# Performance work log

Measured on AMD Instinct MI355X. Metric: run time of the kernel, lower is better.

Reference implementation:

```python
import math
import jax, jax.numpy as jnp
import numpy as np

# Frozen random shifts from the original module's __init__ (random.randint(-1,1))
SHIFT_C = 1   # p_2_0_1: roll along channel dim
SHIFT_H = 1   # p_4_1_0: roll along h
SHIFT_W = -1  # p_4_1_1: roll along w
K = 7         # horizontal window size (F.unfold kernel (1,7), padding (0,3))


def setup_inputs() -> dict:
    key = jax.random.key(0)
    k1, k2 = jax.random.split(key)
    n, c, h, w = 8, 256, 56, 56
    x = jax.random.normal(k1, (n, c, h, w), dtype=jnp.float32)
    # p_1_w ~ trunc_normal(std=0.1) around 1.0; approximate with 1 + 0.1*normal
    p1w = 1.0 + 0.1 * jax.random.normal(k2, (1, c, h, w), dtype=jnp.float32)
    return {"x": x, "p1w": p1w}


def _unfold_w7(t):
    # t: (n,c,h,w) -> (n,c,7,h,w): 7 horizontal taps, zero-padded (pad=3)
    w = t.shape[-1]
    tp = jnp.pad(t, ((0, 0), (0, 0), (0, 0), (3, 3)))
    return jnp.stack([tp[..., j:j + w] for j in range(K)], axis=2)


def reference(x, p1w):
    n, c, h, w = x.shape
    hw = h * w
    t1 = p1w * x                              # (n,c,h,w)
    t2 = jnp.roll(t1, SHIFT_C, axis=1)        # roll channels
    t3 = _unfold_w7(t2)                       # (n,c,7,h,w)
    t4 = jnp.roll(jnp.roll(t3, SHIFT_H, axis=3), SHIFT_W, axis=4)
    t5 = t1[:, :, None] - t3                  # (n,c,7,h,w)
    t6 = x[:, :, None] + t4                   # (n,c,7,h,w)
    x2 = x.reshape(n, c, hw)
    t5r = t5.reshape(n, c, K, hw)
    t6r = t6.reshape(n, c, K, hw)
    # scores: bmm(x (n,c,hw), t5^T (n,hw,c*7)) -> (n,c,c,7)
    t7 = jnp.einsum('nip,njkp->nijk', x2, t5r) / math.sqrt(hw)
    # aggregate: bmm(t7 (n,c,c*7), t6 (n,c*7,hw)) -> (n,c,hw)
    t8 = jnp.einsum('nijk,njkp->nip', t7, t6r) / math.sqrt(c * K)
    return t8.reshape(n, c, h, w)
```

## Files before the change

kernel.cpp:

```cpp
#include <hip/hip_runtime.h>

typedef unsigned short u16;
typedef __bf16 bf16x8 __attribute__((ext_vector_type(8)));
typedef float f32x4 __attribute__((ext_vector_type(4)));

#define HH  56
#define WW  56
#define HW  3136
#define CC  256
#define NB  8
#define CKP 2048
#define KS1 4

__device__ __forceinline__ u16 f2bf(float f) {
  unsigned int u = __float_as_uint(f);
  u += 0x7fffu + ((u >> 16) & 1u);
  return (u16)(u >> 16);
}
__device__ __forceinline__ float bf2f(u16 v) {
  return __uint_as_float((unsigned)v << 16);
}

__device__ __forceinline__ void lds_load16(const void* g, void* l) {
  __builtin_amdgcn_global_load_lds(
      (const __attribute__((address_space(1))) void*)g,
      (__attribute__((address_space(3))) void*)l, 16, 0, 0);
}

__global__ void pass1(const float* __restrict__ x, const float* __restrict__ p1w,
                      u16* __restrict__ t1b, u16* __restrict__ xb) {
  int i = blockIdx.x * 256 + threadIdx.x;
  int cw = i % (CC * HW / 4);
  float4 xv = ((const float4*)x)[i];
  float4 wv = ((const float4*)p1w)[cw];
  uint2 xo = make_uint2((unsigned)f2bf(xv.x) | ((unsigned)f2bf(xv.y) << 16),
                        (unsigned)f2bf(xv.z) | ((unsigned)f2bf(xv.w) << 16));
  ((uint2*)xb)[i] = xo;
  uint2 to = make_uint2((unsigned)f2bf(xv.x * wv.x) | ((unsigned)f2bf(xv.y * wv.y) << 16),
                        (unsigned)f2bf(xv.z * wv.z) | ((unsigned)f2bf(xv.w * wv.w) << 16));
  ((uint2*)t1b)[i] = to;
}

__global__ __launch_bounds__(256)
void gemm1f(const u16* __restrict__ A, const u16* __restrict__ t1b,
            float* __restrict__ Cp) {
  __shared__ u16 As[128 * 64];
  __shared__ u16 Bs[128 * 64];

  const int bi = blockIdx.x;
  const int nb = bi & 7;
  const int r  = bi >> 3;
  const int ks = r & 3;
  const int r2 = r >> 2;
  const int m0b = r2 & 1;
  const int n0b = r2 >> 1;

  const int it0 = 49 * ks / KS1, it1 = 49 * (ks + 1) / KS1;
  const u16* Ab  = A   + (long)nb * CC * HW;
  const u16* t1n = t1b + (long)nb * CC * HW;
  const int m0 = m0b * 128, n0 = n0b * 128;
  const int jb = n0b * 16;
  const int t = threadIdx.x;
  const int lane = t & 63, wave = t >> 6;
  const int wm = wave & 1, wn = wave >> 1;
  const int lm = lane & 15, quad = lane >> 4;

  const int jl = (t >> 3) & 15, pc = t & 7, hf = t >> 7;
  const int j  = jb + jl;
  const int jm = (j + CC - 1) & (CC - 1);
  const u16* arow = t1n + (long)j  * HW;
  const u16* wrow = t1n + (long)jm * HW;

  f32x4 acc[4][4];
#pragma unroll
  for (int a = 0; a < 4; ++a)
#pragma unroll
    for (int b = 0; b < 4; ++b) acc[a][b] = (f32x4)0.0f;

  int rowc[4], colc[4];
#pragma unroll
  for (int ci = 0; ci < 4; ++ci) {
    int c = t + ci * 256;
    rowc[ci] = c >> 3;
    colc[ci] = ((c & 7) ^ (rowc[ci] & 7)) * 8;
  }

  for (int it = it0; it < it1; ++it) {
    const int k0 = it * 64;
#pragma unroll
    for (int ci = 0; ci < 4; ++ci)
      lds_load16(Ab + (long)(m0 + rowc[ci]) * HW + k0 + colc[ci],
                 &As[(t + ci * 256) * 8]);

    {
      const int p8 = k0 + pc * 8;
      __attribute__((aligned(16))) u16 Ar[8];
      __attribute__((aligned(16))) u16 Wd[24];
      *(uint4*)Ar = *(const uint4*)&arow[p8];
#pragma unroll
      for (int L = 0; L < 3; ++L) {
        int ad = p8 - 8 + L * 8;
        ad = ad < 0 ? 0 : (ad > HW - 8 ? HW - 8 : ad);
        *(uint4*)&Wd[L * 8] = *(const uint4*)&wrow[ad];
      }
      const int w0t = p8 % 56;
      int wv[8];
#pragma unroll
      for (int e = 0; e < 8; ++e) { int w = w0t + e; wv[e] = w >= 56 ? w - 56 : w; }
      if (hf == 0) {
#pragma unroll
        for (int k = 0; k < 4; ++k) {
          __attribute__((aligned(16))) u16 v[8];
#pragma unroll
          for (int e = 0; e < 8; ++e)
            v[e] = ((unsigned)(wv[e] + k - 3) < 56u) ? Wd[e + k + 5] : (u16)0;
          *(uint4*)&Bs[(jl * 8 + k) * 64 + (pc ^ k) * 8] = *(const uint4*)v;
        }
      } else {
#pragma unroll
        for (int k = 4; k < 7; ++k) {
          __attribute__((aligned(16))) u16 v[8];
#pragma unroll
          for (int e = 0; e < 8; ++e)
            v[e] = ((unsigned)(wv[e] + k - 3) < 56u) ? Wd[e + k + 5] : (u16)0;
          *(uint4*)&Bs[(jl * 8 + k) * 64 + (pc ^ k) * 8] = *(const uint4*)v;
        }
        *(uint4*)&Bs[(jl * 8 + 7) * 64 + (pc ^ 7) * 8] = *(const uint4*)Ar;
      }
    }
    __syncthreads();
#pragma unroll
    for (int kk = 0; kk < 2; ++kk) {
      const int phys = ((kk * 4 + quad) ^ (lm & 7)) * 8;
      bf16x8 af[4], bv[4];
#pragma unroll
      for (int mi = 0; mi < 4; ++mi)
        af[mi] = *(const bf16x8*)&As[(wm * 64 + mi * 16 + lm) * 64 + phys];
#pragma unroll
      for (int ni = 0; ni < 4; ++ni)
        bv[ni] = *(const bf16x8*)&Bs[(wn * 64 + ni * 16 + lm) * 64 + phys];
#pragma unroll
      for (int mi = 0; mi < 4; ++mi)
#pragma unroll
        for (int ni = 0; ni < 4; ++ni)
          acc[mi][ni] = __builtin_amdgcn_mfma_f32_16x16x32_bf16(
              af[mi], bv[ni], acc[mi][ni], 0, 0, 0);
    }
    __syncthreads();
  }

  float* Cb = Cp + ((long)ks * NB + nb) * (long)CC * CKP;
#pragma unroll
  for (int mi = 0; mi < 4; ++mi)
#pragma unroll
    for (int ni = 0; ni < 4; ++ni) {
      int rb = m0 + wm * 64 + mi * 16 + quad * 4;
      int cg = n0 + wn * 64 + ni * 16 + lm;
#pragma unroll
      for (int r4 = 0; r4 < 4; ++r4)
        Cb[(long)(rb + r4) * CKP + cg] = acc[mi][ni][r4];
    }
}

__global__ void reduce1(const float* __restrict__ p1, u16* __restrict__ t7) {
  const int g = blockIdx.x * 256 + threadIdx.x;
  const long S = (long)NB * CC * CKP;
  const long base = (long)g * 8;
  float a[8];
#pragma unroll
  for (int e = 0; e < 8; ++e) a[e] = 0.0f;
#pragma unroll
  for (int ks = 0; ks < KS1; ++ks) {
    float4 lo = *(const float4*)&p1[ks * S + base];
    float4 hi = *(const float4*)&p1[ks * S + base + 4];
    a[0] += lo.x; a[1] += lo.y; a[2] += lo.z; a[3] += lo.w;
    a[4] += hi.x; a[5] += hi.y; a[6] += hi.z; a[7] += hi.w;
  }
  const float s = 1.0f / 56.0f;
  const float G = a[7];
  __attribute__((aligned(16))) u16 o[8];
  float s7 = 0.0f;
#pragma unroll
  for (int k = 0; k < 7; ++k) {
    float v = (G - a[k]) * s;
    s7 += v;
    o[k] = f2bf(v);
  }
  o[7] = f2bf(s7);
  *(uint4*)&t7[base] = *(const uint4*)o;
}

__global__ __launch_bounds__(256)
void gemm2f(const u16* __restrict__ A, const u16* __restrict__ xb,
            const u16* __restrict__ t1b, float* __restrict__ out) {
  __shared__ u16 As[128 * 64];
  __shared__ u16 Bs[64 * 64];

  const int bi = blockIdx.x;
  const int nb = bi & 7;
  const int r  = bi >> 3;
  const int m0b = r & 1;
  const int n0b = r >> 1;

  const u16* Ab  = A   + (long)nb * CC * CKP;
  const u16* xbn = xb  + (long)nb * CC * HW;
  const u16* t1n = t1b + (long)nb * CC * HW;
  const int m0 = m0b * 128, n0 = n0b * 64;
  const int t = threadIdx.x;
  const int lane = t & 63, wave = t >> 6;
  const int wm = wave & 1, wn = wave >> 1;
  const int lm = lane & 15, quad = lane >> 4;

  const int pr = t & 63, jg = t >> 6;
  const int p  = n0 + pr;
  const int h  = p / WW, w = p - h * WW;
  const int h2 = (h + HH - 1) % HH;
  const int w2 = (w + 1) % WW;
  const int swz = pr & 7;

  int toff[7], tmsk[7];
#pragma unroll
  for (int k = 0; k < 7; ++k) {
    int ww = w2 + k - 3;
    int wc = ww < 0 ? 0 : (ww > 55 ? 55 : ww);
    toff[k] = h2 * WW + wc;
    tmsk[k] = ((unsigned)ww < 56u);
  }

  f32x4 acc[4][2];
#pragma unroll
  for (int a = 0; a < 4; ++a)
#pragma unroll
    for (int b = 0; b < 2; ++b) acc[a][b] = (f32x4)0.0f;

  int rowc[4], colc[4];
#pragma unroll
  for (int ci = 0; ci < 4; ++ci) {
    int c = t + ci * 256;
    rowc[ci] = c >> 3;
    colc[ci] = ((c & 7) ^ (rowc[ci] & 7)) * 8;
  }

  for (int it = 0; it < 32; ++it) {
    const int k0 = it * 64;
#pragma unroll
    for (int ci = 0; ci < 4; ++ci)
      lds_load16(Ab + (long)(m0 + rowc[ci]) * CKP + k0 + colc[ci],
                 &As[(t + ci * 256) * 8]);

#pragma unroll
    for (int jj = 0; jj < 2; ++jj) {
      const int jch = it * 8 + jg * 2 + jj;
      const int jmm = (jch + CC - 1) & (CC - 1);
      const u16* trow = t1n + (long)jmm * HW;
      __attribute__((aligned(16))) u16 v[8];
#pragma unroll
      for (int k = 0; k < 7; ++k) {
        u16 tv = trow[toff[k]];
        v[k] = tmsk[k] ? tv : (u16)0;
      }
      v[7] = xbn[(long)jch * HW + p];
      *(uint4*)&Bs[pr * 64 + (((jg * 2 + jj) ^ swz) * 8)] = *(const uint4*)v;
    }
    __syncthreads();
#pragma unroll
    for (int kk = 0; kk < 2; ++kk) {
      const int phys = ((kk * 4 + quad) ^ (lm & 7)) * 8;
      bf16x8 af[4], bv[2];
#pragma unroll
      for (int mi = 0; mi < 4; ++mi)
        af[mi] = *(const bf16x8*)&As[(wm * 64 + mi * 16 + lm) * 64 + phys];
#pragma unroll
      for (int ni = 0; ni < 2; ++ni)
        bv[ni] = *(const bf16x8*)&Bs[(wn * 32 + ni * 16 + lm) * 64 + phys];
#pragma unroll
      for (int mi = 0; mi < 4; ++mi)
#pragma unroll
        for (int ni = 0; ni < 2; ++ni)
          acc[mi][ni] = __builtin_amdgcn_mfma_f32_16x16x32_bf16(
              af[mi], bv[ni], acc[mi][ni], 0, 0, 0);
    }
    __syncthreads();
  }

  const float s2 = 0.023622783f;
  float* Ob = out + (long)nb * CC * HW;
#pragma unroll
  for (int mi = 0; mi < 4; ++mi)
#pragma unroll
    for (int ni = 0; ni < 2; ++ni) {
      int rb = m0 + wm * 64 + mi * 16 + quad * 4;
      int cg = n0 + wn * 32 + ni * 16 + lm;
#pragma unroll
      for (int r4 = 0; r4 < 4; ++r4)
        Ob[(long)(rb + r4) * HW + cg] = acc[mi][ni][r4] * s2;
    }
}

extern "C" void kernel_launch(void* const* d_in, const int* in_sizes, int n_in,
                              void* d_out, int out_size, void* d_ws, size_t ws_size,
                              hipStream_t stream) {
  const float* x   = (const float*)d_in[0];
  const float* p1w = (const float*)d_in[1];

  char* ws = (char*)d_ws;
  size_t o = 0;
  u16* xb  = (u16*)(ws + o); o += (size_t)NB * CC * HW * 2;
  u16* t1b = (u16*)(ws + o); o += (size_t)NB * CC * HW * 2;
  u16* t7  = (u16*)(ws + o); o += (size_t)NB * CC * CKP * 2;
  float* p1 = (float*)(ws + o); o += (size_t)KS1 * NB * CC * CKP * 4;

  pass1<<<NB * CC * HW / 4 / 256, 256, 0, stream>>>(x, p1w, t1b, xb);
  gemm1f<<<NB * KS1 * 2 * 16, 256, 0, stream>>>(xb, t1b, p1);
  reduce1<<<NB * CC * CKP / 8 / 256, 256, 0, stream>>>(p1, t7);
  gemm2f<<<NB * 2 * 49, 256, 0, stream>>>(t7, xb, t1b, (float*)d_out);
}
```

Before: 185.6 us.

## Stage t1/x rows into double-buffered LDS via async DMA in gemm2f

Instead of each thread doing seven scattered 2-byte global loads per channel to build the unfolded B tile, two waves asynchronously copy the two needed source rows of t1 and the x slice into LDS with global_load_lds. The stage for the next iteration is double-buffered, and the B tile is then assembled from LDS. This is meant to replace uncoalesced global gathers with coalesced 16-byte DMA and to overlap them with compute. The cost is more LDS, more complex indexing that assumes a 64-pixel tile spans at most two image rows, and possible LDS bank conflicts during the gather.

New measurement: 177.8 us. 1.04x faster.

```diff
diff --git a/kernel.cpp b/kernel.cpp
--- a/kernel.cpp
+++ b/kernel.cpp
@@ -195,6 +195,8 @@
             const u16* __restrict__ t1b, float* __restrict__ out) {
   __shared__ u16 As[128 * 64];
   __shared__ u16 Bs[64 * 64];
+  __shared__ __attribute__((aligned(16))) u16 Rs0[896], Rs1[896];
+  __shared__ __attribute__((aligned(16))) u16 Xs0[512], Xs1[512];
 
   const int bi = blockIdx.x;
   const int nb = bi & 7;
@@ -214,17 +216,40 @@
   const int pr = t & 63, jg = t >> 6;
   const int p  = n0 + pr;
   const int h  = p / WW, w = p - h * WW;
-  const int h2 = (h + HH - 1) % HH;
   const int w2 = (w + 1) % WW;
   const int swz = pr & 7;
-
-  int toff[7], tmsk[7];
+  const int h_lo = n0 / WW;
+  const int slot = h - h_lo;
+
+  int roff[2][7], rmsk[7];
 #pragma unroll
   for (int k = 0; k < 7; ++k) {
     int ww = w2 + k - 3;
     int wc = ww < 0 ? 0 : (ww > 55 ? 55 : ww);
-    toff[k] = h2 * WW + wc;
-    tmsk[k] = ((unsigned)ww < 56u);
+    rmsk[k] = ((unsigned)ww < 56u);
+#pragma unroll
+    for (int jj = 0; jj < 2; ++jj)
+      roff[jj][k] = ((jg * 2 + jj) * 2 + slot) * 56 + wc;
+  }
+  const int xoff0 = (jg * 2 + 0) * 64 + pr;
+  const int xoff1 = (jg * 2 + 1) * 64 + pr;
+
+  long stSrcOff = 0;
+  int  stCh = 0;
+  bool stR = false, stX = false;
+  {
+    if (wave == 1) {
+      stX = true; stCh = lane >> 3;
+      stSrcOff = n0 + (lane & 7) * 8;
+    } else if (wave == 2 || (wave == 3 && lane < 48)) {
+      stR = true;
+      int c = (wave == 2) ? lane : 64 + lane;
+      stCh = c / 14;
+      int rem = c - stCh * 14;
+      int s = rem / 7, i = rem - s * 7;
+      int h2s = ((h_lo + s) + HH - 1) % HH;
+      stSrcOff = h2s * 56 + i * 8;
+    }
   }
 
   f32x4 acc[4][2];
@@ -241,47 +266,78 @@
     colc[ci] = ((c & 7) ^ (rowc[ci] & 7)) * 8;
   }
 
-  for (int it = 0; it < 32; ++it) {
-    const int k0 = it * 64;
-#pragma unroll
-    for (int ci = 0; ci < 4; ++ci)
-      lds_load16(Ab + (long)(m0 + rowc[ci]) * CKP + k0 + colc[ci],
-                 &As[(t + ci * 256) * 8]);
-
-#pragma unroll
-    for (int jj = 0; jj < 2; ++jj) {
-      const int jch = it * 8 + jg * 2 + jj;
-      const int jmm = (jch + CC - 1) & (CC - 1);
-      const u16* trow = t1n + (long)jmm * HW;
-      __attribute__((aligned(16))) u16 v[8];
-#pragma unroll
-      for (int k = 0; k < 7; ++k) {
-        u16 tv = trow[toff[k]];
-        v[k] = tmsk[k] ? tv : (u16)0;
-      }
-      v[7] = xbn[(long)jch * HW + p];
-      *(uint4*)&Bs[pr * 64 + (((jg * 2 + jj) ^ swz) * 8)] = *(const uint4*)v;
-    }
-    __syncthreads();
-#pragma unroll
-    for (int kk = 0; kk < 2; ++kk) {
-      const int phys = ((kk * 4 + quad) ^ (lm & 7)) * 8;
-      bf16x8 af[4], bv[2];
-#pragma unroll
-      for (int mi = 0; mi < 4; ++mi)
-        af[mi] = *(const bf16x8*)&As[(wm * 64 + mi * 16 + lm) * 64 + phys];
-#pragma unroll
-      for (int ni = 0; ni < 2; ++ni)
-        bv[ni] = *(const bf16x8*)&Bs[(wn * 32 + ni * 16 + lm) * 64 + phys];
-#pragma unroll
-      for (int mi = 0; mi < 4; ++mi)
-#pragma unroll
-        for (int ni = 0; ni < 2; ++ni)
-          acc[mi][ni] = __builtin_amdgcn_mfma_f32_16x16x32_bf16(
-              af[mi], bv[ni], acc[mi][ni], 0, 0, 0);
-    }
-    __syncthreads();
-  }
+#define DMAA(itn) do { const int k0_ = (itn) * 64;                             \
+    _Pragma("unroll")                                                          \
+    for (int ci = 0; ci < 4; ++ci)                                             \
+      lds_load16(Ab + (long)(m0 + rowc[ci]) * CKP + k0_ + colc[ci],            \
+                 &As[(t + ci * 256) * 8]); } while (0)
+
+#define STAGE(RsD, XsD, itn) do {                                              \
+    if (stX)                                                                   \
+      lds_load16(xbn + (long)((itn) * 8 + stCh) * HW + stSrcOff,               \
+                 &XsD[lane * 8]);                                              \
+    else if (stR) {                                                            \
+      const int jmm_ = ((itn) * 8 + stCh + CC - 1) & (CC - 1);                 \
+      lds_load16(t1n + (long)jmm_ * HW + stSrcOff,                             \
+                 (wave == 2) ? &RsD[lane * 8] : &RsD[512 + lane * 8]);         \
+    } } while (0)
+
+#define BGEN(RsS, XsS) do {                                                    \
+    __attribute__((aligned(16))) u16 v0[8], v1[8];                             \
+    _Pragma("unroll")                                                          \
+    for (int k = 0; k < 7; ++k) {                                              \
+      u16 a_ = RsS[roff[0][k]], b_ = RsS[roff[1][k]];                          \
+      v0[k] = rmsk[k] ? a_ : (u16)0;                                           \
+      v1[k] = rmsk[k] ? b_ : (u16)0;                                           \
+    }                                                                          \
+    v0[7] = XsS[xoff0];                                                        \
+    v1[7] = XsS[xoff1];                                                        \
+    *(uint4*)&Bs[pr * 64 + (((jg * 2 + 0) ^ swz) * 8)] = *(const uint4*)v0;    \
+    *(uint4*)&Bs[pr * 64 + (((jg * 2 + 1) ^ swz) * 8)] = *(const uint4*)v1;    \
+  } while (0)
+
+#define MFMA2(void0) do {                                                      \
+    _Pragma("unroll")                                                          \
+    for (int kk = 0; kk < 2; ++kk) {                                           \
+      const int phys = ((kk * 4 + quad) ^ (lm & 7)) * 8;                       \
+      bf16x8 af[4], bv[2];                                                     \
+      _Pragma("unroll")                                                        \
+      for (int mi = 0; mi < 4; ++mi)                                           \
+        af[mi] = *(const bf16x8*)&As[(wm * 64 + mi * 16 + lm) * 64 + phys];    \
+      _Pragma("unroll")                                                        \
+      for (int ni = 0; ni < 2; ++ni)                                           \
+        bv[ni] = *(const bf16x8*)&Bs[(wn * 32 + ni * 16 + lm) * 64 + phys];    \
+      _Pragma("unroll")                                                        \
+      for (int mi = 0; mi < 4; ++mi)                                           \
+        _Pragma("unroll")                                                      \
+        for (int ni = 0; ni < 2; ++ni)                                         \
+          acc[mi][ni] = __builtin_amdgcn_mfma_f32_16x16x32_bf16(               \
+              af[mi], bv[ni], acc[mi][ni], 0, 0, 0);                           \
+    } } while (0)
+
+  STAGE(Rs0, Xs0, 0);
+  __syncthreads();
+
+  for (int itp = 0; itp < 16; ++itp) {
+    const int itE = itp * 2;
+    DMAA(itE);
+    STAGE(Rs1, Xs1, itE + 1);
+    BGEN(Rs0, Xs0);
+    __syncthreads();
+    MFMA2();
+    __syncthreads();
+    DMAA(itE + 1);
+    if (itE + 2 < 32) STAGE(Rs0, Xs0, itE + 2);
+    BGEN(Rs1, Xs1);
+    __syncthreads();
+    MFMA2();
+    __syncthreads();
+  }
+
+#undef DMAA
+#undef STAGE
+#undef BGEN
+#undef MFMA2
 
   const float s2 = 0.023622783f;
   float* Ob = out + (long)nb * CC * HW;
```
